# Kernel optimization log

Measured on AMD Instinct MI355X. Metric: run time of the kernel, lower is better.

Reference implementation:

```python
import jax, jax.numpy as jnp
import numpy as np

DIM = 768
HEADS = 12


def setup_inputs() -> dict:
    key = jax.random.key(0)
    ks = jax.random.split(key, 8)
    B, N, C = 4, 1024, DIM
    x = jax.random.normal(ks[0], (B, N, C), dtype=jnp.float32)
    mask = jax.random.normal(ks[1], (B, 1, N, N), dtype=jnp.float32)
    weight = jax.random.uniform(ks[2], (B, N), dtype=jnp.float32)
    s = 1.0 / np.sqrt(C)
    qkv_w = jax.random.normal(ks[3], (3 * C, C), dtype=jnp.float32) * s
    mu_w = jax.random.normal(ks[4], (C, C // 2), dtype=jnp.float32) * s
    mu_b = jnp.zeros((C,), dtype=jnp.float32)
    ls_w = jax.random.normal(ks[5], (C, C // 2), dtype=jnp.float32) * s
    ls_b = jnp.zeros((C,), dtype=jnp.float32)
    return {"x": x, "mask": mask, "weight": weight, "qkv_w": qkv_w,
            "mu_w": mu_w, "mu_b": mu_b, "ls_w": ls_w, "ls_b": ls_b}


def reference(x, mask, weight, qkv_w, mu_w, mu_b, ls_w, ls_b):
    B, N, C = x.shape
    H = HEADS
    Dh = C // H
    # NOTE: module uses head_dim = dim * num_heads for the scale (quirk, kept faithful)
    scale = (C * H) ** (-0.5)
    qkv = (x @ qkv_w.T).reshape(B, N, 3, H, Dh).transpose(2, 0, 3, 1, 4)  # [3,B,H,N,Dh]
    q, k, v = qkv[0], qkv[1], qkv[2]
    attn = jnp.einsum('bhnd,bhmd->bhnm', q, k) * scale + mask  # [B,H,N,N]
    attn = jax.nn.softmax(attn, axis=-1)
    # weight: [B,N] broadcast over heads and queries (key axis)
    w = weight[:, None, None, :] + 1e-10
    attn = attn * w
    attn = attn / attn.sum(axis=-1, keepdims=True)
    out = jnp.einsum('bhnm,bhmd->bhnd', attn, v)          # [B,H,N,Dh]
    out = out.transpose(0, 2, 1, 3).reshape(B, N, C)      # [B,N,C]
    mu_in = out[:, :, :C // 2]
    ls_in = out[:, :, C // 2:]
    mu = mu_in @ mu_w.T + mu_b
    logsigma = ls_in @ ls_w.T + ls_b
    return (mu, logsigma, attn)
```

## Files before the change

### kernel.cpp

```cpp
#include <hip/hip_runtime.h>
#include <hip/hip_bf16.h>

typedef __attribute__((ext_vector_type(8))) short short8;
typedef __attribute__((ext_vector_type(4))) float f32x4;
typedef __attribute__((ext_vector_type(4))) unsigned short u16x4;

#define NB 4
#define NN 1024
#define NC 768
#define NH 12
#define TC 2304

#define OFF_XB   0ul
#define OFF_WQ   6291456ul
#define OFF_WMU  (OFF_WQ + 3538944ul)
#define OFF_WLS  (OFF_WMU + 589824ul)
#define OFF_QKVB (OFF_WLS + 589824ul)
#define OFF_V3   (OFF_QKVB + 18874368ul)
#define OFF_OUTB (OFF_V3 + 6291456ul)

__device__ __forceinline__ unsigned short f2bf(float f) {
    unsigned int u = __float_as_uint(f);
    u = (u + 0x7FFFu + ((u >> 16) & 1u)) >> 16;
    return (unsigned short)u;
}

__device__ __forceinline__ void gload_lds16(const unsigned short* g, unsigned short* l) {
    __builtin_amdgcn_global_load_lds(
        (const __attribute__((address_space(1))) unsigned int*)g,
        (__attribute__((address_space(3))) unsigned int*)l, 16, 0, 0);
}

__device__ __forceinline__ void gload16(short8& dst, const unsigned short* p) {
    asm volatile("global_load_dwordx4 %0, %1, off" : "=v"(dst) : "v"(p));
}
#define WAITV(N) do { asm volatile("s_waitcnt vmcnt(" #N ")" ::: "memory"); \
                      __builtin_amdgcn_sched_barrier(0); } while (0)
#define SBAR()   __builtin_amdgcn_sched_barrier(0)

__global__ void cast_all(const float* __restrict__ x, const float* __restrict__ qkv_w,
                         const float* __restrict__ mu_w, const float* __restrict__ ls_w,
                         unsigned short* __restrict__ dst) {
    int i = blockIdx.x * blockDim.x + threadIdx.x;
    const float* src; int off;
    if (i < 786432)            { src = x;     off = i; }
    else if (i < 1228800)      { src = qkv_w; off = i - 786432; }
    else if (i < 1302528)      { src = mu_w;  off = i - 1228800; }
    else                       { src = ls_w;  off = i - 1302528; }
    f32x4 v = ((const f32x4*)src)[off];
    u16x4 o;
#pragma unroll
    for (int j = 0; j < 4; ++j) o[j] = f2bf(v[j]);
    ((u16x4*)dst)[i] = o;
}

template <int EPI>
__device__ __forceinline__ void gemm_body(
    unsigned short* As, unsigned short* Bs,
    const unsigned short* __restrict__ A, const unsigned short* __restrict__ Bm,
    int K, int lda, int ldb, void* __restrict__ Cout, int ldc,
    const float* __restrict__ bias, int row0, int col0)
{
    const int t = threadIdx.x;
    const int lane = t & 63;
    const int wv = t >> 6;
    const int wm = wv >> 1, wn = wv & 1;
    const int li = lane & 15;
    const int koff = (lane >> 4) * 8;

    f32x4 acc[4][4] = {};

    const int tr = t >> 2;
    const int tc = (t & 3) * 8;
    const unsigned short* ag = A + (size_t)(row0 + tr) * lda + tc;
    const unsigned short* bg = Bm + (size_t)(col0 + tr) * ldb + tc;

    for (int kt = 0; kt < K; kt += 32) {
        gload_lds16(ag,            As + t * 8);
        gload_lds16(ag + 64 * lda, As + 2048 + t * 8);
        gload_lds16(bg,            Bs + t * 8);
        gload_lds16(bg + 64 * ldb, Bs + 2048 + t * 8);
        ag += 32; bg += 32;
        __syncthreads();
        short8 af[4], bf[4];
#pragma unroll
        for (int m = 0; m < 4; ++m)
            af[m] = *(const short8*)&As[(wm * 64 + m * 16 + li) * 32 + koff];
#pragma unroll
        for (int n = 0; n < 4; ++n)
            bf[n] = *(const short8*)&Bs[(wn * 64 + n * 16 + li) * 32 + koff];
#pragma unroll
        for (int m = 0; m < 4; ++m)
#pragma unroll
            for (int n = 0; n < 4; ++n)
                acc[m][n] = __builtin_amdgcn_mfma_f32_16x16x32_bf16(af[m], bf[n], acc[m][n], 0, 0, 0);
        __syncthreads();
    }

#pragma unroll
    for (int m = 0; m < 4; ++m) {
        const int row = row0 + wm * 64 + m * 16 + (lane >> 4) * 4;
#pragma unroll
        for (int n = 0; n < 4; ++n) {
            const int col = col0 + wn * 64 + n * 16 + li;
#pragma unroll
            for (int r = 0; r < 4; ++r) {
                if (EPI == 0) {
                    ((unsigned short*)Cout)[(size_t)(row + r) * ldc + col] = f2bf(acc[m][n][r]);
                } else {
                    ((float*)Cout)[(size_t)(row + r) * ldc + col] = acc[m][n][r] + bias[col];
                }
            }
        }
    }
}

__global__ __launch_bounds__(256, 2) void gemm_qkv(
    const unsigned short* __restrict__ A, const unsigned short* __restrict__ Bm,
    unsigned short* __restrict__ C)
{
    __shared__ unsigned short As[128 * 32];
    __shared__ unsigned short Bs[128 * 32];
    const int bid = blockIdx.y * gridDim.x + blockIdx.x;
    const int nwg = gridDim.x * gridDim.y;
    const int swz = (bid & 7) * (nwg >> 3) + (bid >> 3);
    const int row0 = (swz / gridDim.x) * 128;
    const int col0 = (swz % gridDim.x) * 128;
    gemm_body<0>(As, Bs, A, Bm, NC, NC, NC, C, TC, nullptr, row0, col0);
}

__global__ __launch_bounds__(256, 2) void gemm_heads(
    const unsigned short* __restrict__ outb,
    const unsigned short* __restrict__ wmu, const unsigned short* __restrict__ wls,
    const float* __restrict__ mu_b, const float* __restrict__ ls_b,
    float* __restrict__ out_mu, float* __restrict__ out_ls)
{
    __shared__ unsigned short As[128 * 32];
    __shared__ unsigned short Bs[128 * 32];
    const int bid = blockIdx.y * gridDim.x + blockIdx.x;
    const int nwg = gridDim.x * gridDim.y;
    const int swz = (bid & 7) * (nwg >> 3) + (bid >> 3);
    const int row0 = (swz / gridDim.x) * 128;
    const int col0 = (swz % gridDim.x) * 128;
    const int z = blockIdx.z;
    gemm_body<1>(As, Bs, outb + (z ? 384 : 0), z ? wls : wmu, 384, NC, 384,
                 z ? (void*)out_ls : (void*)out_mu, NC, z ? ls_b : mu_b, row0, col0);
}

__global__ __launch_bounds__(256, 4) void pack_v(
    const unsigned short* __restrict__ qkvb, unsigned short* __restrict__ v3)
{
    __shared__ unsigned short tile[64][65];
    const int t = threadIdx.x;
    const int bh = blockIdx.y;
    const int b = bh / NH, h = bh % NH;
    const int m0 = blockIdx.x * 64;
#pragma unroll
    for (int i = 0; i < 2; ++i) {
        int lin = i * 256 + t;
        int mr = lin >> 3;
        int dr = (lin & 7) * 8;
        short8 v = *(const short8*)(qkvb + (size_t)(b * NN + m0 + mr) * TC + 1536 + h * 64 + dr);
#pragma unroll
        for (int j = 0; j < 8; ++j) tile[mr][dr + j] = (unsigned short)v[j];
    }
    __syncthreads();
#pragma unroll
    for (int i = 0; i < 2; ++i) {
        int lin = i * 256 + t;
        int dw = lin >> 3;
        int mw = (lin & 7) * 8;
        short8 v;
#pragma unroll
        for (int j = 0; j < 8; ++j) v[j] = (short)tile[mw + j][dw];
        int kt = (m0 + mw) >> 5;
        int mm = mw & 31;
        *(short8*)(v3 + ((size_t)(bh * 32 + kt) * 64 + dw) * 32 + mm) = v;
    }
}

__global__ __launch_bounds__(512, 6) void attn_kernel(
    const unsigned short* __restrict__ qkvb, const unsigned short* __restrict__ v3,
    const float* __restrict__ mask, const float* __restrict__ weight,
    float* __restrict__ attn_out, unsigned short* __restrict__ outb)
{
    __shared__ __align__(16) char smem[33024];
    __shared__ f32x4 po[4][64];
    __shared__ float red_max[8][16];
    __shared__ float red_sum[8][16];

    const int t = threadIdx.x;
    const int lane = t & 63;
    const int wv = t >> 6;
    const int li = lane & 15;
    const int g = lane >> 4;
    const int koff = g * 8;
    const int bh = blockIdx.y;
    const int b = bh / NH, h = bh % NH;
    const int n0 = blockIdx.x * 16;

    unsigned short* sm = (unsigned short*)smem;

    const unsigned short* qp = qkvb + (size_t)(b * NN + n0 + li) * TC + h * 64 + koff;
    short8 qf0 = *(const short8*)qp;
    short8 qf1 = *(const short8*)(qp + 32);

    const float* mrow = mask + (size_t)b * NN * NN + (size_t)(n0 + li) * NN + wv * 16 + g * 4;
    const unsigned short* kgbase = qkvb + (size_t)(b * NN) * TC + 768 + h * 64;

    f32x4 acc[8];
    f32x4 mk[2];

    auto stage = [&](int ck) {
#pragma unroll
        for (int i = 0; i < 2; ++i) {
            int m = wv * 16 + i * 8 + (lane >> 3);
            int sl = (lane & 7) ^ (m & 7);
            const unsigned short* src = kgbase + (size_t)(ck * 128 + m) * TC + sl * 8;
            unsigned short* dst = sm + (ck & 1) * 8192 + wv * 1024 + i * 512 + lane * 8;
            gload_lds16(src, dst);
        }
    };

    stage(0);
    mk[0] = *(const f32x4*)(mrow);
    __syncthreads();

#pragma unroll
    for (int ck = 0; ck < 8; ++ck) {
        if (ck < 7) {
            stage(ck + 1);
            mk[(ck + 1) & 1] = *(const f32x4*)(mrow + (ck + 1) * 128);
        }
        const unsigned short* kbuf = sm + (ck & 1) * 8192;
        short8 kf0 = *(const short8*)&kbuf[(wv * 16 + li) * 64 + ((g ^ (li & 7)) * 8)];
        short8 kf1 = *(const short8*)&kbuf[(wv * 16 + li) * 64 + (((g + 4) ^ (li & 7)) * 8)];
        f32x4 ci = mk[ck & 1] * 96.0f;
        ci = __builtin_amdgcn_mfma_f32_16x16x32_bf16(kf0, qf0, ci, 0, 0, 0);
        ci = __builtin_amdgcn_mfma_f32_16x16x32_bf16(kf1, qf1, ci, 0, 0, 0);
        acc[ck] = ci;
        __syncthreads();
    }

    const float scale = 1.0f / 96.0f;
    float rmax = -1e30f;
#pragma unroll
    for (int cf = 0; cf < 8; ++cf) {
#pragma unroll
        for (int r = 0; r < 4; ++r) rmax = fmaxf(rmax, acc[cf][r]);
    }
    rmax = fmaxf(rmax, __shfl_xor(rmax, 16, 64));
    rmax = fmaxf(rmax, __shfl_xor(rmax, 32, 64));
    if (lane < 16) red_max[wv][lane] = rmax;
    __syncthreads();
    {
        float m01 = fmaxf(red_max[0][li], red_max[1][li]);
        float m23 = fmaxf(red_max[2][li], red_max[3][li]);
        float m45 = fmaxf(red_max[4][li], red_max[5][li]);
        float m67 = fmaxf(red_max[6][li], red_max[7][li]);
        rmax = fmaxf(fmaxf(m01, m23), fmaxf(m45, m67)) * scale;
    }

    unsigned short (*P)[1032] = (unsigned short(*)[1032])smem;
    const float* wbase = weight + b * NN + wv * 16 + g * 4;
    float rsum = 0.f;
#pragma unroll
    for (int cf = 0; cf < 8; ++cf) {
        f32x4 wcf = *(const f32x4*)(wbase + cf * 128);
        u16x4 pb;
#pragma unroll
        for (int r = 0; r < 4; ++r) {
            float p = __expf(acc[cf][r] * scale - rmax) * (wcf[r] + 1e-10f);
            acc[cf][r] = p;
            rsum += p;
            pb[r] = f2bf(p);
        }
        *(u16x4*)&P[li][cf * 128 + wv * 16 + g * 4] = pb;
    }
    rsum += __shfl_xor(rsum, 16, 64);
    rsum += __shfl_xor(rsum, 32, 64);
    if (lane < 16) red_sum[wv][lane] = rsum;
    __syncthreads();

    const float rinv = 1.0f / (red_sum[0][li] + red_sum[1][li] + red_sum[2][li]
                             + red_sum[3][li] + red_sum[4][li] + red_sum[5][li]
                             + red_sum[6][li] + red_sum[7][li]);
    float* arow = attn_out + (size_t)bh * NN * NN + (size_t)(n0 + li) * NN + wv * 16 + g * 4;
#pragma unroll
    for (int cf = 0; cf < 8; ++cf) {
        f32x4 a4;
#pragma unroll
        for (int r = 0; r < 4; ++r) a4[r] = acc[cf][r] * rinv;
        __builtin_nontemporal_store(a4, (f32x4*)(arow + cf * 128));
    }

    const int kh = wv >> 2, p4 = wv & 3;
    f32x4 o = {};
    const unsigned short* v3s = v3 + (size_t)bh * 65536 + (size_t)(kh * 16) * 2048
                              + p4 * 512 + li * 32 + g * 8;
    short8 vA[4], vB[4];
#define VISSUE(c, vb2) do {                                                   \
        _Pragma("unroll")                                                     \
        for (int j2 = 0; j2 < 4; ++j2) gload16(vb2[j2], v3s + ((c) * 4 + j2) * 2048); \
    } while (0)
#define VCOMP(c, vb2) do {                                                    \
        __builtin_amdgcn_s_setprio(1);                                        \
        _Pragma("unroll")                                                     \
        for (int j2 = 0; j2 < 4; ++j2) {                                      \
            const int kt = kh * 16 + (c) * 4 + j2;                            \
            short8 pa = *(const short8*)&P[li][kt * 32 + koff];               \
            o = __builtin_amdgcn_mfma_f32_16x16x32_bf16(pa, vb2[j2], o, 0, 0, 0); \
        }                                                                     \
        __builtin_amdgcn_s_setprio(0);                                        \
    } while (0)
    VISSUE(0, vA);
    VISSUE(1, vB);
    WAITV(4);  VCOMP(0, vA); SBAR(); VISSUE(2, vA);
    WAITV(4);  VCOMP(1, vB); SBAR(); VISSUE(3, vB);
    WAITV(4);  VCOMP(2, vA);
    WAITV(0);  VCOMP(3, vB);
#undef VISSUE
#undef VCOMP

    if (kh == 1) po[p4][lane] = o;
    __syncthreads();
    if (kh == 0) {
        f32x4 oo = po[p4][lane];
        const int dcol = h * 64 + p4 * 16 + li;
#pragma unroll
        for (int r = 0; r < 4; ++r) {
            const int row = g * 4 + r;
            const float rs = red_sum[0][row] + red_sum[1][row] + red_sum[2][row]
                           + red_sum[3][row] + red_sum[4][row] + red_sum[5][row]
                           + red_sum[6][row] + red_sum[7][row];
            outb[(size_t)(b * NN + n0 + row) * NC + dcol] = f2bf((o[r] + oo[r]) / rs);
        }
    }
}

extern "C" void kernel_launch(void* const* d_in, const int* in_sizes, int n_in,
                              void* d_out, int out_size, void* d_ws, size_t ws_size,
                              hipStream_t stream) {
    const float* x      = (const float*)d_in[0];
    const float* mask   = (const float*)d_in[1];
    const float* weight = (const float*)d_in[2];
    const float* qkv_w  = (const float*)d_in[3];
    const float* mu_w   = (const float*)d_in[4];
    const float* mu_b   = (const float*)d_in[5];
    const float* ls_w   = (const float*)d_in[6];
    const float* ls_b   = (const float*)d_in[7];

    char* ws = (char*)d_ws;
    unsigned short* xb   = (unsigned short*)(ws + OFF_XB);
    unsigned short* wq   = (unsigned short*)(ws + OFF_WQ);
    unsigned short* wmu  = (unsigned short*)(ws + OFF_WMU);
    unsigned short* wls  = (unsigned short*)(ws + OFF_WLS);
    unsigned short* qkvb = (unsigned short*)(ws + OFF_QKVB);
    unsigned short* v3   = (unsigned short*)(ws + OFF_V3);
    unsigned short* outb = (unsigned short*)(ws + OFF_OUTB);

    float* out_mu   = (float*)d_out;
    float* out_ls   = out_mu + 3145728;
    float* out_attn = out_mu + 6291456;

    cast_all<<<5376, 256, 0, stream>>>(x, qkv_w, mu_w, ls_w, xb);

    gemm_qkv<<<dim3(TC / 128, 4096 / 128), 256, 0, stream>>>(xb, wq, qkvb);

    pack_v<<<dim3(NN / 64, NB * NH), 256, 0, stream>>>(qkvb, v3);

    attn_kernel<<<dim3(NN / 16, NB * NH), 512, 0, stream>>>(
        qkvb, v3, mask, weight, out_attn, outb);

    gemm_heads<<<dim3(NC / 128, 4096 / 128, 2), 256, 0, stream>>>(
        outb, wmu, wls, mu_b, ls_b, out_mu, out_ls);
}
```

Before: 144.7 us.

## Fuse V repacking into QKV GEMM epilogue and pipeline attention K loads

The separate pack_v kernel is removed. The QKV GEMM epilogue now writes the V columns directly in the transposed, tiled v3 layout, which saves one launch and one round trip of V through memory. The attention QK^T loop drops its per-chunk __syncthreads. In its place it keeps two chunks of K and mask loads in flight and waits on explicit vmcnt counters, relying on each wave touching only its own LDS rows. The cost is that the fused epilogue issues scattered 2-byte stores for V, and the hand-counted waits become fragile if the number of issued loads changes.

```diff
diff --git a/kernel.cpp b/kernel.cpp
--- a/kernel.cpp
+++ b/kernel.cpp
@@ -32,6 +32,9 @@
 }
 
 __device__ __forceinline__ void gload16(short8& dst, const unsigned short* p) {
+    asm volatile("global_load_dwordx4 %0, %1, off" : "=v"(dst) : "v"(p));
+}
+__device__ __forceinline__ void gloadf4(f32x4& dst, const float* p) {
     asm volatile("global_load_dwordx4 %0, %1, off" : "=v"(dst) : "v"(p));
 }
 #define WAITV(N) do { asm volatile("s_waitcnt vmcnt(" #N ")" ::: "memory"); \
@@ -59,7 +62,8 @@
     unsigned short* As, unsigned short* Bs,
     const unsigned short* __restrict__ A, const unsigned short* __restrict__ Bm,
     int K, int lda, int ldb, void* __restrict__ Cout, int ldc,
-    const float* __restrict__ bias, int row0, int col0)
+    const float* __restrict__ bias, int row0, int col0,
+    unsigned short* __restrict__ v3)
 {
     const int t = threadIdx.x;
     const int lane = t & 63;
@@ -105,10 +109,20 @@
             const int col = col0 + wn * 64 + n * 16 + li;
 #pragma unroll
             for (int r = 0; r < 4; ++r) {
-                if (EPI == 0) {
-                    ((unsigned short*)Cout)[(size_t)(row + r) * ldc + col] = f2bf(acc[m][n][r]);
+                if (EPI == 1) {
+                    ((float*)Cout)[(size_t)(row + r) * ldc + col] = acc[m][n][r] + bias[col];
                 } else {
-                    ((float*)Cout)[(size_t)(row + r) * ldc + col] = acc[m][n][r] + bias[col];
+                    unsigned short bv = f2bf(acc[m][n][r]);
+                    if (col0 >= 1536) {
+                        const int rr = row + r;
+                        const int b_ = rr >> 10, n_ = rr & 1023;
+                        const int hd = col - 1536;
+                        const int bh_ = b_ * NH + (hd >> 6);
+                        const int d_ = hd & 63;
+                        v3[(((size_t)bh_ * 32 + (n_ >> 5)) * 64 + d_) * 32 + (n_ & 31)] = bv;
+                    } else {
+                        ((unsigned short*)Cout)[(size_t)(row + r) * ldc + col] = bv;
+                    }
                 }
             }
         }
@@ -117,7 +131,7 @@
 
 __global__ __launch_bounds__(256, 2) void gemm_qkv(
     const unsigned short* __restrict__ A, const unsigned short* __restrict__ Bm,
-    unsigned short* __restrict__ C)
+    unsigned short* __restrict__ C, unsigned short* __restrict__ v3)
 {
     __shared__ unsigned short As[128 * 32];
     __shared__ unsigned short Bs[128 * 32];
@@ -126,7 +140,7 @@
     const int swz = (bid & 7) * (nwg >> 3) + (bid >> 3);
     const int row0 = (swz / gridDim.x) * 128;
     const int col0 = (swz % gridDim.x) * 128;
-    gemm_body<0>(As, Bs, A, Bm, NC, NC, NC, C, TC, nullptr, row0, col0);
+    gemm_body<2>(As, Bs, A, Bm, NC, NC, NC, C, TC, nullptr, row0, col0, v3);
 }
 
 __global__ __launch_bounds__(256, 2) void gemm_heads(
@@ -144,39 +158,7 @@
     const int col0 = (swz % gridDim.x) * 128;
     const int z = blockIdx.z;
     gemm_body<1>(As, Bs, outb + (z ? 384 : 0), z ? wls : wmu, 384, NC, 384,
-                 z ? (void*)out_ls : (void*)out_mu, NC, z ? ls_b : mu_b, row0, col0);
-}
-
-__global__ __launch_bounds__(256, 4) void pack_v(
-    const unsigned short* __restrict__ qkvb, unsigned short* __restrict__ v3)
-{
-    __shared__ unsigned short tile[64][65];
-    const int t = threadIdx.x;
-    const int bh = blockIdx.y;
-    const int b = bh / NH, h = bh % NH;
-    const int m0 = blockIdx.x * 64;
-#pragma unroll
-    for (int i = 0; i < 2; ++i) {
-        int lin = i * 256 + t;
-        int mr = lin >> 3;
-        int dr = (lin & 7) * 8;
-        short8 v = *(const short8*)(qkvb + (size_t)(b * NN + m0 + mr) * TC + 1536 + h * 64 + dr);
-#pragma unroll
-        for (int j = 0; j < 8; ++j) tile[mr][dr + j] = (unsigned short)v[j];
-    }
-    __syncthreads();
-#pragma unroll
-    for (int i = 0; i < 2; ++i) {
-        int lin = i * 256 + t;
-        int dw = lin >> 3;
-        int mw = (lin & 7) * 8;
-        short8 v;
-#pragma unroll
-        for (int j = 0; j < 8; ++j) v[j] = (short)tile[mw + j][dw];
-        int kt = (m0 + mw) >> 5;
-        int mm = mw & 31;
-        *(short8*)(v3 + ((size_t)(bh * 32 + kt) * 64 + dw) * 32 + mm) = v;
-    }
+                 z ? (void*)out_ls : (void*)out_mu, NC, z ? ls_b : mu_b, row0, col0, nullptr);
 }
 
 __global__ __launch_bounds__(512, 6) void attn_kernel(
@@ -201,46 +183,50 @@
 
     unsigned short* sm = (unsigned short*)smem;
 
-    const unsigned short* qp = qkvb + (size_t)(b * NN + n0 + li) * TC + h * 64 + koff;
-    short8 qf0 = *(const short8*)qp;
-    short8 qf1 = *(const short8*)(qp + 32);
-
     const float* mrow = mask + (size_t)b * NN * NN + (size_t)(n0 + li) * NN + wv * 16 + g * 4;
     const unsigned short* kgbase = qkvb + (size_t)(b * NN) * TC + 768 + h * 64;
 
+    const unsigned short* qp = qkvb + (size_t)(b * NN + n0 + li) * TC + h * 64 + koff;
+    short8 qf0, qf1;
+    gload16(qf0, qp);
+    gload16(qf1, qp + 32);
+
     f32x4 acc[8];
     f32x4 mk[2];
 
-    auto stage = [&](int ck) {
-#pragma unroll
-        for (int i = 0; i < 2; ++i) {
-            int m = wv * 16 + i * 8 + (lane >> 3);
-            int sl = (lane & 7) ^ (m & 7);
-            const unsigned short* src = kgbase + (size_t)(ck * 128 + m) * TC + sl * 8;
-            unsigned short* dst = sm + (ck & 1) * 8192 + wv * 1024 + i * 512 + lane * 8;
-            gload_lds16(src, dst);
-        }
-    };
-
-    stage(0);
-    mk[0] = *(const f32x4*)(mrow);
-    __syncthreads();
-
-#pragma unroll
-    for (int ck = 0; ck < 8; ++ck) {
-        if (ck < 7) {
-            stage(ck + 1);
-            mk[(ck + 1) & 1] = *(const f32x4*)(mrow + (ck + 1) * 128);
-        }
-        const unsigned short* kbuf = sm + (ck & 1) * 8192;
-        short8 kf0 = *(const short8*)&kbuf[(wv * 16 + li) * 64 + ((g ^ (li & 7)) * 8)];
-        short8 kf1 = *(const short8*)&kbuf[(wv * 16 + li) * 64 + (((g + 4) ^ (li & 7)) * 8)];
-        f32x4 ci = mk[ck & 1] * 96.0f;
-        ci = __builtin_amdgcn_mfma_f32_16x16x32_bf16(kf0, qf0, ci, 0, 0, 0);
-        ci = __builtin_amdgcn_mfma_f32_16x16x32_bf16(kf1, qf1, ci, 0, 0, 0);
-        acc[ck] = ci;
-        __syncthreads();
-    }
+#define KISSUE(c) do {                                                        \
+        _Pragma("unroll")                                                     \
+        for (int i_ = 0; i_ < 2; ++i_) {                                      \
+            int m_ = wv * 16 + i_ * 8 + (lane >> 3);                          \
+            int sl_ = (lane & 7) ^ (m_ & 7);                                  \
+            const unsigned short* src_ = kgbase + (size_t)((c) * 128 + m_) * TC + sl_ * 8; \
+            unsigned short* dst_ = sm + ((c) & 1) * 8192 + wv * 1024 + i_ * 512 + lane * 8; \
+            gload_lds16(src_, dst_);                                          \
+        }                                                                     \
+        gloadf4(mk[(c) & 1], mrow + (c) * 128);                               \
+    } while (0)
+
+#define KSTEP(c) do {                                                         \
+        const unsigned short* kbuf_ = sm + ((c) & 1) * 8192;                  \
+        short8 kf0 = *(const short8*)&kbuf_[(wv * 16 + li) * 64 + ((g ^ (li & 7)) * 8)];       \
+        short8 kf1 = *(const short8*)&kbuf_[(wv * 16 + li) * 64 + (((g + 4) ^ (li & 7)) * 8)]; \
+        f32x4 ci = mk[(c) & 1] * 96.0f;                                       \
+        ci = __builtin_amdgcn_mfma_f32_16x16x32_bf16(kf0, qf0, ci, 0, 0, 0);  \
+        ci = __builtin_amdgcn_mfma_f32_16x16x32_bf16(kf1, qf1, ci, 0, 0, 0);  \
+        acc[(c)] = ci;                                                        \
+    } while (0)
+
+    KISSUE(0); KISSUE(1);
+    WAITV(3);  KSTEP(0); SBAR(); KISSUE(2);
+    WAITV(3);  KSTEP(1); SBAR(); KISSUE(3);
+    WAITV(3);  KSTEP(2); SBAR(); KISSUE(4);
+    WAITV(3);  KSTEP(3); SBAR(); KISSUE(5);
+    WAITV(3);  KSTEP(4); SBAR(); KISSUE(6);
+    WAITV(3);  KSTEP(5); SBAR(); KISSUE(7);
+    WAITV(3);  KSTEP(6);
+    WAITV(0);  KSTEP(7);
+#undef KISSUE
+#undef KSTEP
 
     const float scale = 1.0f / 96.0f;
     float rmax = -1e30f;
@@ -365,9 +351,7 @@
 
     cast_all<<<5376, 256, 0, stream>>>(x, qkv_w, mu_w, ls_w, xb);
 
-    gemm_qkv<<<dim3(TC / 128, 4096 / 128), 256, 0, stream>>>(xb, wq, qkvb);
-
-    pack_v<<<dim3(NN / 64, NB * NH), 256, 0, stream>>>(qkvb, v3);
+    gemm_qkv<<<dim3(TC / 128, 4096 / 128), 256, 0, stream>>>(xb, wq, qkvb, v3);
 
     attn_kernel<<<dim3(NN / 16, NB * NH), 512, 0, stream>>>(
         qkvb, v3, mask, weight, out_attn, outb);
```

Measured after the change: 148.6 us. 1.03x slower.
